# Performance work log

Hardware: AMD Instinct MI355X
Metric: run time of the kernel (lower is better)

The kernel has to match this reference:

```python
import jax, jax.numpy as jnp
import numpy as np

N = 50000
E = 1600000
IN_DIM = 128
HEADS = 4
OUT_DIM = 32
NEG_SLOPE = 0.2


def setup_inputs() -> dict:
    key = jax.random.key(0)
    k1, k2, k3, k4, k5, k6 = jax.random.split(key, 6)
    x = jax.random.normal(k1, (N, IN_DIM), dtype=jnp.float32)
    src = jax.random.randint(k2, (E,), 0, N)
    dst = jax.random.randint(k3, (E,), 0, N)
    edge_index = jnp.stack([src, dst], axis=0).astype(jnp.int64)
    W = jax.random.normal(k4, (IN_DIM, HEADS * OUT_DIM), dtype=jnp.float32) * 0.08
    att = jax.random.normal(k5, (HEADS, 2 * OUT_DIM), dtype=jnp.float32) * 0.1
    bias = jnp.zeros((HEADS * OUT_DIM,), dtype=jnp.float32)
    return {"x": x, "edge_index": edge_index, "W": W, "att": att, "bias": bias}


def reference(x, edge_index, W, att, bias):
    src, dst = edge_index[0], edge_index[1]
    n = x.shape[0]
    # Linear projection -> [N, H, F]
    Wh = (x @ W).reshape(n, HEADS, OUT_DIM)
    # Per-node attention score halves (equivalent to (cat[Wh_i,Wh_j]*att).sum(-1))
    a_src = jnp.einsum("nhf,hf->nh", Wh, att[:, :OUT_DIM])  # [N, H]
    a_dst = jnp.einsum("nhf,hf->nh", Wh, att[:, OUT_DIM:])  # [N, H]
    logits = jax.nn.leaky_relu(a_src[src] + a_dst[dst], negative_slope=NEG_SLOPE)  # [E, H]
    # Segment softmax over destination nodes (numerically stable)
    seg_max = jax.ops.segment_max(logits, dst, num_segments=n)  # [N, H]
    exp_s = jnp.exp(logits - seg_max[dst])
    denom = jnp.clip(jax.ops.segment_sum(exp_s, dst, num_segments=n), 1e-9, None)
    alpha = exp_s / denom[dst]  # [E, H]
    # Weighted messages from SOURCE features, scatter-sum to destinations
    messages = alpha[:, :, None] * Wh[src]  # [E, H, F]
    out = jax.ops.segment_sum(messages.reshape(-1, HEADS * OUT_DIM), dst, num_segments=n)
    return out + bias
```

## Files before the change

kernel.cpp:

```cpp
#include <hip/hip_runtime.h>
#include <hip/hip_fp16.h>
#include <math.h>

#define N_NODES 50000
#define E_EDGES 1600000
#define IN_DIM 128
#define HEADS 4
#define OUT_DIM 32
#define HF 128
#define NEG_SLOPE 0.2f
#define NBUCK 196
#define BCAP 8800

__global__ __launch_bounds__(256) void gat_proj(
        const float* __restrict__ x, const float* __restrict__ W,
        const float* __restrict__ att, __half* __restrict__ Whh,
        float* __restrict__ a_src, float* __restrict__ a_dst) {
    __shared__ float Ws[IN_DIM][HF];
    __shared__ float xs[64][132];
    __shared__ float atts[HEADS][2 * OUT_DIM];

    const int tid = threadIdx.x;

    const float4* W4 = (const float4*)W;
    float4* Ws4 = (float4*)&Ws[0][0];
#pragma unroll
    for (int i = 0; i < 16; ++i) Ws4[tid + 256 * i] = W4[tid + 256 * i];
    if (tid < 64) ((float4*)&atts[0][0])[tid] = ((const float4*)att)[tid];

    const int rowBase = blockIdx.x * 64;
    const int rowsHere = min(64, N_NODES - rowBase);
    const float4* x4 = (const float4*)(x + (size_t)rowBase * IN_DIM);
    for (int i = tid; i < rowsHere * 32; i += 256) {
        const int r = i >> 5, q = i & 31;
        *(float4*)&xs[r][q * 4] = x4[i];
    }
    __syncthreads();

    const int rg = tid >> 4;
    const int cg = tid & 15;
    const int r0 = rg * 4;
    const int c0 = cg * 8;
    const int h  = cg >> 2;
    const int f0 = (cg & 3) * 8;

    float acc[4][8];
#pragma unroll
    for (int i = 0; i < 4; ++i)
#pragma unroll
        for (int j = 0; j < 8; ++j) acc[i][j] = 0.f;

    for (int k0 = 0; k0 < IN_DIM; k0 += 4) {
        float4 a4[4];
#pragma unroll
        for (int i = 0; i < 4; ++i) a4[i] = *(const float4*)&xs[r0 + i][k0];
#pragma unroll
        for (int kk = 0; kk < 4; ++kk) {
            float4 w0 = *(const float4*)&Ws[k0 + kk][c0];
            float4 w1 = *(const float4*)&Ws[k0 + kk][c0 + 4];
            const float wv[8] = {w0.x, w0.y, w0.z, w0.w, w1.x, w1.y, w1.z, w1.w};
            const float av[4] = {(&a4[0].x)[kk], (&a4[1].x)[kk],
                                 (&a4[2].x)[kk], (&a4[3].x)[kk]};
#pragma unroll
            for (int j = 0; j < 8; ++j) {
                acc[0][j] = fmaf(av[0], wv[j], acc[0][j]);
                acc[1][j] = fmaf(av[1], wv[j], acc[1][j]);
                acc[2][j] = fmaf(av[2], wv[j], acc[2][j]);
                acc[3][j] = fmaf(av[3], wv[j], acc[3][j]);
            }
        }
    }

#pragma unroll
    for (int i = 0; i < 4; ++i) {
        const int r = r0 + i;
        if (r >= rowsHere) break;
        const int row = rowBase + r;
        union { __half2 h[4]; float4 f; } u;
        u.h[0] = __floats2half2_rn(acc[i][0], acc[i][1]);
        u.h[1] = __floats2half2_rn(acc[i][2], acc[i][3]);
        u.h[2] = __floats2half2_rn(acc[i][4], acc[i][5]);
        u.h[3] = __floats2half2_rn(acc[i][6], acc[i][7]);
        *(float4*)(Whh + (size_t)row * HF + c0) = u.f;

        float ps = 0.f, pd = 0.f;
#pragma unroll
        for (int j = 0; j < 8; ++j) {
            ps = fmaf(acc[i][j], atts[h][f0 + j], ps);
            pd = fmaf(acc[i][j], atts[h][OUT_DIM + f0 + j], pd);
        }
        ps += __shfl_xor(ps, 1, 64); ps += __shfl_xor(ps, 2, 64);
        pd += __shfl_xor(pd, 1, 64); pd += __shfl_xor(pd, 2, 64);
        if ((cg & 3) == 0) {
            a_src[row * HEADS + h] = ps;
            a_dst[row * HEADS + h] = pd;
        }
    }
}

__global__ __launch_bounds__(256) void gat_p1(
        const int* __restrict__ ei, int* __restrict__ gCount,
        unsigned int* __restrict__ gBuck) {
    __shared__ int hist[NBUCK];
    __shared__ int cur[NBUCK];
    const int t = threadIdx.x;
    for (int i = t; i < NBUCK; i += 256) hist[i] = 0;
    __syncthreads();

    unsigned int keys[16];
    bool valid[4];
    const int base4 = blockIdx.x * 1024 + t;
#pragma unroll
    for (int j = 0; j < 4; ++j) {
        const int i4 = base4 + 256 * j;
        valid[j] = (i4 < E_EDGES / 4);
        if (valid[j]) {
            const int4 s4 = ((const int4*)ei)[i4];
            const int4 d4 = ((const int4*)(ei + E_EDGES))[i4];
            keys[j * 4 + 0] = ((unsigned)d4.x << 16) | (unsigned)s4.x;
            keys[j * 4 + 1] = ((unsigned)d4.y << 16) | (unsigned)s4.y;
            keys[j * 4 + 2] = ((unsigned)d4.z << 16) | (unsigned)s4.z;
            keys[j * 4 + 3] = ((unsigned)d4.w << 16) | (unsigned)s4.w;
#pragma unroll
            for (int q = 0; q < 4; ++q)
                atomicAdd(&hist[keys[j * 4 + q] >> 24], 1);
        }
    }
    __syncthreads();
    for (int i = t; i < NBUCK; i += 256)
        cur[i] = atomicAdd(&gCount[i], hist[i]);
    __syncthreads();
#pragma unroll
    for (int j = 0; j < 4; ++j) {
        if (!valid[j]) continue;
#pragma unroll
        for (int q = 0; q < 4; ++q) {
            const unsigned int k = keys[j * 4 + q];
            const int b = k >> 24;
            const int p = atomicAdd(&cur[b], 1);
            if (p < BCAP) gBuck[(size_t)b * BCAP + p] = k;
        }
    }
}

__global__ __launch_bounds__(256) void gat_p2(
        const int* __restrict__ gCount, const unsigned int* __restrict__ gBuck,
        unsigned short* __restrict__ csr, int* __restrict__ offsets) {
    __shared__ int pre[256];
    __shared__ int hist[256];
    __shared__ int loc[256];
    __shared__ unsigned short out16[BCAP];
    const int b = blockIdx.x;
    const int t = threadIdx.x;

    int v = (t < NBUCK) ? min(gCount[t], BCAP) : 0;
    pre[t] = v;
    __syncthreads();
#pragma unroll
    for (int d = 1; d < 256; d <<= 1) {
        int u = (t >= d) ? pre[t - d] : 0;
        __syncthreads();
        pre[t] += u;
        __syncthreads();
    }
    const int total = pre[255];
    const int baseb = (b > 0) ? pre[b - 1] : 0;
    const int cnt = min(gCount[b], BCAP);

    hist[t] = 0;
    __syncthreads();
    for (int i = t; i < cnt; i += 256)
        atomicAdd(&hist[(gBuck[(size_t)b * BCAP + i] >> 16) & 255], 1);
    __syncthreads();
    const int hv = hist[t];
    loc[t] = hv;
    __syncthreads();
#pragma unroll
    for (int d = 1; d < 256; d <<= 1) {
        int u = (t >= d) ? loc[t - d] : 0;
        __syncthreads();
        loc[t] += u;
        __syncthreads();
    }
    const int myloc = loc[t] - hv;
    const int node = b * 256 + t;
    if (node < N_NODES) offsets[node] = baseb + myloc;
    if (b == 0 && t == 0) offsets[N_NODES] = total;
    __syncthreads();

    hist[t] = myloc;
    __syncthreads();
    for (int i = t; i < cnt; i += 256) {
        const unsigned int k = gBuck[(size_t)b * BCAP + i];
        const int n = (k >> 16) & 255;
        const int r = atomicAdd(&hist[n], 1);
        out16[r] = (unsigned short)(k & 0xFFFFu);
    }
    __syncthreads();
    for (int i = t; i < cnt; i += 256)
        csr[baseb + i] = out16[i];
}

__global__ __launch_bounds__(256) void gat_gather(
        const int* __restrict__ offsets, const unsigned short* __restrict__ csr,
        const float* __restrict__ a_src, const float* __restrict__ a_dst,
        const __half* __restrict__ Whh, const float* __restrict__ bias,
        float* __restrict__ out) {
    const int node = blockIdx.x * 4 + (threadIdx.x >> 6);
    const int lane = threadIdx.x & 63;
    if (node >= N_NODES) return;
    const int h = lane >> 4;
    const float ad = a_dst[node * HEADS + h];
    const __half2* __restrict__ Wh2 = (const __half2*)Whh;

    float accx = 0.f, accy = 0.f, den = 0.f;
    const int beg = offsets[node];
    const int end = offsets[node + 1];
    const int cnt = end - beg;

    for (int base = 0; base < cnt; base += 64) {
        const int rem = min(64, cnt - base);
        const int idx = (base + lane < cnt) ? (int)csr[beg + base + lane] : 0;
        int j = 0;
        for (; j + 4 <= rem; j += 4) {
            const int s0 = __shfl(idx, j,     64);
            const int s1 = __shfl(idx, j + 1, 64);
            const int s2 = __shfl(idx, j + 2, 64);
            const int s3 = __shfl(idx, j + 3, 64);
            const float as0 = a_src[s0 * 4 + h];
            const float as1 = a_src[s1 * 4 + h];
            const float as2 = a_src[s2 * 4 + h];
            const float as3 = a_src[s3 * 4 + h];
            const __half2 v0 = Wh2[(size_t)s0 * 64 + lane];
            const __half2 v1 = Wh2[(size_t)s1 * 64 + lane];
            const __half2 v2 = Wh2[(size_t)s2 * 64 + lane];
            const __half2 v3 = Wh2[(size_t)s3 * 64 + lane];
            float t0 = as0 + ad; t0 = fmaxf(t0, NEG_SLOPE * t0);
            float t1 = as1 + ad; t1 = fmaxf(t1, NEG_SLOPE * t1);
            float t2 = as2 + ad; t2 = fmaxf(t2, NEG_SLOPE * t2);
            float t3 = as3 + ad; t3 = fmaxf(t3, NEG_SLOPE * t3);
            const float w0 = __expf(t0), w1 = __expf(t1);
            const float w2 = __expf(t2), w3 = __expf(t3);
            const float2 f0 = __half22float2(v0);
            const float2 f1 = __half22float2(v1);
            const float2 f2 = __half22float2(v2);
            const float2 f3 = __half22float2(v3);
            accx = fmaf(w0, f0.x, accx); accy = fmaf(w0, f0.y, accy);
            accx = fmaf(w1, f1.x, accx); accy = fmaf(w1, f1.y, accy);
            accx = fmaf(w2, f2.x, accx); accy = fmaf(w2, f2.y, accy);
            accx = fmaf(w3, f3.x, accx); accy = fmaf(w3, f3.y, accy);
            den += w0 + w1 + w2 + w3;
        }
        for (; j < rem; ++j) {
            const int s = __shfl(idx, j, 64);
            float t = a_src[s * 4 + h] + ad;
            t = fmaxf(t, NEG_SLOPE * t);
            const float w = __expf(t);
            const float2 v = __half22float2(Wh2[(size_t)s * 64 + lane]);
            accx = fmaf(w, v.x, accx);
            accy = fmaf(w, v.y, accy);
            den += w;
        }
    }
    const float inv = 1.f / fmaxf(den, 1e-9f);
    const float2 b2 = ((const float2*)bias)[lane];
    float2 o = {accx * inv + b2.x, accy * inv + b2.y};
    ((float2*)out)[(size_t)node * 64 + lane] = o;
}

extern "C" void kernel_launch(void* const* d_in, const int* in_sizes, int n_in,
                              void* d_out, int out_size, void* d_ws, size_t ws_size,
                              hipStream_t stream) {
    const float* x    = (const float*)d_in[0];
    const int*   ei   = (const int*)d_in[1];
    const float* W    = (const float*)d_in[2];
    const float* att  = (const float*)d_in[3];
    const float* bias = (const float*)d_in[4];
    float* out = (float*)d_out;

    __half* Whh   = (__half*)d_ws;
    float* a_src  = (float*)(Whh + (size_t)N_NODES * HF);
    float* a_dst  = a_src + (size_t)N_NODES * HEADS;
    unsigned int* gBuck = (unsigned int*)(a_dst + (size_t)N_NODES * HEADS);
    unsigned short* csr = (unsigned short*)(gBuck + (size_t)NBUCK * BCAP);
    int*   offsets = (int*)(csr + (size_t)E_EDGES);
    int*   gCount  = offsets + N_NODES + 8;

    hipMemsetAsync(gCount, 0, NBUCK * sizeof(int), stream);
    gat_proj<<<(N_NODES + 63) / 64, 256, 0, stream>>>(x, W, att, Whh, a_src, a_dst);
    gat_p1<<<(E_EDGES / 4 + 1023) / 1024, 256, 0, stream>>>(ei, gCount, gBuck);
    gat_p2<<<NBUCK, 256, 0, stream>>>(gCount, gBuck, csr, offsets);
    gat_gather<<<(N_NODES + 3) / 4, 256, 0, stream>>>(offsets, csr, a_src,
                                                      a_dst, Whh, bias, out);
}
```

Baseline: 223.3 us.

## Deduplicate per-edge softmax weights across lanes and halve projection shared memory

In the gather kernel, each 16-lane head group now computes the attention weight for 16 edges at once, one edge per lane, and broadcasts the weights with shuffles. Before, every lane recomputed the a_src load, leaky-relu and exp for every edge, so this removes 16x redundant transcendental work and scattered loads. The denominator is then reduced across the 16 lanes with xor-shuffles. Separately, the projection kernel stages W in two 64-row halves, cutting its shared memory footprint to allow more blocks per CU, at the cost of extra barriers.

```diff
diff --git a/kernel.cpp b/kernel.cpp
--- a/kernel.cpp
+++ b/kernel.cpp
@@ -16,16 +16,11 @@
         const float* __restrict__ x, const float* __restrict__ W,
         const float* __restrict__ att, __half* __restrict__ Whh,
         float* __restrict__ a_src, float* __restrict__ a_dst) {
-    __shared__ float Ws[IN_DIM][HF];
+    __shared__ float Ws[64][HF];
     __shared__ float xs[64][132];
     __shared__ float atts[HEADS][2 * OUT_DIM];
 
     const int tid = threadIdx.x;
-
-    const float4* W4 = (const float4*)W;
-    float4* Ws4 = (float4*)&Ws[0][0];
-#pragma unroll
-    for (int i = 0; i < 16; ++i) Ws4[tid + 256 * i] = W4[tid + 256 * i];
     if (tid < 64) ((float4*)&atts[0][0])[tid] = ((const float4*)att)[tid];
 
     const int rowBase = blockIdx.x * 64;
@@ -35,7 +30,6 @@
         const int r = i >> 5, q = i & 31;
         *(float4*)&xs[r][q * 4] = x4[i];
     }
-    __syncthreads();
 
     const int rg = tid >> 4;
     const int cg = tid & 15;
@@ -50,23 +44,36 @@
 #pragma unroll
         for (int j = 0; j < 8; ++j) acc[i][j] = 0.f;
 
-    for (int k0 = 0; k0 < IN_DIM; k0 += 4) {
-        float4 a4[4];
-#pragma unroll
-        for (int i = 0; i < 4; ++i) a4[i] = *(const float4*)&xs[r0 + i][k0];
-#pragma unroll
-        for (int kk = 0; kk < 4; ++kk) {
-            float4 w0 = *(const float4*)&Ws[k0 + kk][c0];
-            float4 w1 = *(const float4*)&Ws[k0 + kk][c0 + 4];
-            const float wv[8] = {w0.x, w0.y, w0.z, w0.w, w1.x, w1.y, w1.z, w1.w};
-            const float av[4] = {(&a4[0].x)[kk], (&a4[1].x)[kk],
-                                 (&a4[2].x)[kk], (&a4[3].x)[kk]};
-#pragma unroll
-            for (int j = 0; j < 8; ++j) {
-                acc[0][j] = fmaf(av[0], wv[j], acc[0][j]);
-                acc[1][j] = fmaf(av[1], wv[j], acc[1][j]);
-                acc[2][j] = fmaf(av[2], wv[j], acc[2][j]);
-                acc[3][j] = fmaf(av[3], wv[j], acc[3][j]);
+    float4* Ws4 = (float4*)&Ws[0][0];
+#pragma unroll
+    for (int half = 0; half < 2; ++half) {
+        __syncthreads();
+        const float4* Wsrc = (const float4*)(W + half * 64 * HF);
+#pragma unroll
+        for (int i = 0; i < 8; ++i) Ws4[tid + 256 * i] = Wsrc[tid + 256 * i];
+        __syncthreads();
+
+        const int kb = half * 64;
+        for (int k0 = 0; k0 < 64; k0 += 4) {
+            float4 a4[4];
+#pragma unroll
+            for (int i = 0; i < 4; ++i)
+                a4[i] = *(const float4*)&xs[r0 + i][kb + k0];
+#pragma unroll
+            for (int kk = 0; kk < 4; ++kk) {
+                float4 w0 = *(const float4*)&Ws[k0 + kk][c0];
+                float4 w1 = *(const float4*)&Ws[k0 + kk][c0 + 4];
+                const float wv[8] = {w0.x, w0.y, w0.z, w0.w,
+                                     w1.x, w1.y, w1.z, w1.w};
+                const float av[4] = {(&a4[0].x)[kk], (&a4[1].x)[kk],
+                                     (&a4[2].x)[kk], (&a4[3].x)[kk]};
+#pragma unroll
+                for (int j = 0; j < 8; ++j) {
+                    acc[0][j] = fmaf(av[0], wv[j], acc[0][j]);
+                    acc[1][j] = fmaf(av[1], wv[j], acc[1][j]);
+                    acc[2][j] = fmaf(av[2], wv[j], acc[2][j]);
+                    acc[3][j] = fmaf(av[3], wv[j], acc[3][j]);
+                }
             }
         }
     }
@@ -210,58 +217,67 @@
     const int lane = threadIdx.x & 63;
     if (node >= N_NODES) return;
     const int h = lane >> 4;
+    const int hbase = lane & 48;
+    const int sub = lane & 15;
     const float ad = a_dst[node * HEADS + h];
     const __half2* __restrict__ Wh2 = (const __half2*)Whh;
 
-    float accx = 0.f, accy = 0.f, den = 0.f;
+    float accx = 0.f, accy = 0.f, denOwn = 0.f;
     const int beg = offsets[node];
-    const int end = offsets[node + 1];
-    const int cnt = end - beg;
+    const int cnt = offsets[node + 1] - beg;
 
     for (int base = 0; base < cnt; base += 64) {
         const int rem = min(64, cnt - base);
         const int idx = (base + lane < cnt) ? (int)csr[beg + base + lane] : 0;
-        int j = 0;
-        for (; j + 4 <= rem; j += 4) {
-            const int s0 = __shfl(idx, j,     64);
-            const int s1 = __shfl(idx, j + 1, 64);
-            const int s2 = __shfl(idx, j + 2, 64);
-            const int s3 = __shfl(idx, j + 3, 64);
-            const float as0 = a_src[s0 * 4 + h];
-            const float as1 = a_src[s1 * 4 + h];
-            const float as2 = a_src[s2 * 4 + h];
-            const float as3 = a_src[s3 * 4 + h];
-            const __half2 v0 = Wh2[(size_t)s0 * 64 + lane];
-            const __half2 v1 = Wh2[(size_t)s1 * 64 + lane];
-            const __half2 v2 = Wh2[(size_t)s2 * 64 + lane];
-            const __half2 v3 = Wh2[(size_t)s3 * 64 + lane];
-            float t0 = as0 + ad; t0 = fmaxf(t0, NEG_SLOPE * t0);
-            float t1 = as1 + ad; t1 = fmaxf(t1, NEG_SLOPE * t1);
-            float t2 = as2 + ad; t2 = fmaxf(t2, NEG_SLOPE * t2);
-            float t3 = as3 + ad; t3 = fmaxf(t3, NEG_SLOPE * t3);
-            const float w0 = __expf(t0), w1 = __expf(t1);
-            const float w2 = __expf(t2), w3 = __expf(t3);
-            const float2 f0 = __half22float2(v0);
-            const float2 f1 = __half22float2(v1);
-            const float2 f2 = __half22float2(v2);
-            const float2 f3 = __half22float2(v3);
-            accx = fmaf(w0, f0.x, accx); accy = fmaf(w0, f0.y, accy);
-            accx = fmaf(w1, f1.x, accx); accy = fmaf(w1, f1.y, accy);
-            accx = fmaf(w2, f2.x, accx); accy = fmaf(w2, f2.y, accy);
-            accx = fmaf(w3, f3.x, accx); accy = fmaf(w3, f3.y, accy);
-            den += w0 + w1 + w2 + w3;
-        }
-        for (; j < rem; ++j) {
-            const int s = __shfl(idx, j, 64);
-            float t = a_src[s * 4 + h] + ad;
+        const int nchunk = (rem + 15) >> 4;
+        for (int cj = 0; cj < nchunk; ++cj) {
+            const int e0 = cj << 4;
+            const int sOwn = __shfl(idx, e0 + sub, 64);
+            float t = a_src[sOwn * 4 + h] + ad;
             t = fmaxf(t, NEG_SLOPE * t);
-            const float w = __expf(t);
-            const float2 v = __half22float2(Wh2[(size_t)s * 64 + lane]);
-            accx = fmaf(w, v.x, accx);
-            accy = fmaf(w, v.y, accy);
-            den += w;
-        }
-    }
+            float wOwn = __expf(t);
+            if (base + e0 + sub >= cnt) wOwn = 0.f;
+            denOwn += wOwn;
+
+            const int jmax = min(16, rem - e0);
+            int j = 0;
+            for (; j + 4 <= jmax; j += 4) {
+                const int s0 = __shfl(idx, e0 + j,     64);
+                const int s1 = __shfl(idx, e0 + j + 1, 64);
+                const int s2 = __shfl(idx, e0 + j + 2, 64);
+                const int s3 = __shfl(idx, e0 + j + 3, 64);
+                const __half2 v0 = Wh2[(size_t)s0 * 64 + lane];
+                const __half2 v1 = Wh2[(size_t)s1 * 64 + lane];
+                const __half2 v2 = Wh2[(size_t)s2 * 64 + lane];
+                const __half2 v3 = Wh2[(size_t)s3 * 64 + lane];
+                const float w0 = __shfl(wOwn, hbase + j,     64);
+                const float w1 = __shfl(wOwn, hbase + j + 1, 64);
+                const float w2 = __shfl(wOwn, hbase + j + 2, 64);
+                const float w3 = __shfl(wOwn, hbase + j + 3, 64);
+                const float2 f0 = __half22float2(v0);
+                const float2 f1 = __half22float2(v1);
+                const float2 f2 = __half22float2(v2);
+                const float2 f3 = __half22float2(v3);
+                accx = fmaf(w0, f0.x, accx); accy = fmaf(w0, f0.y, accy);
+                accx = fmaf(w1, f1.x, accx); accy = fmaf(w1, f1.y, accy);
+                accx = fmaf(w2, f2.x, accx); accy = fmaf(w2, f2.y, accy);
+                accx = fmaf(w3, f3.x, accx); accy = fmaf(w3, f3.y, accy);
+            }
+            for (; j < jmax; ++j) {
+                const int s = __shfl(idx, e0 + j, 64);
+                const float w = __shfl(wOwn, hbase + j, 64);
+                const float2 v = __half22float2(Wh2[(size_t)s * 64 + lane]);
+                accx = fmaf(w, v.x, accx);
+                accy = fmaf(w, v.y, accy);
+            }
+        }
+    }
+    float den = denOwn;
+    den += __shfl_xor(den, 1, 64);
+    den += __shfl_xor(den, 2, 64);
+    den += __shfl_xor(den, 4, 64);
+    den += __shfl_xor(den, 8, 64);
+
     const float inv = 1.f / fmaxf(den, 1e-9f);
     const float2 b2 = ((const float2*)bias)[lane];
     float2 o = {accx * inv + b2.x, accy * inv + b2.y};
```

Measured after the change: 210.0 us. 1.06x faster.
